# Optimization experiments

Measured on AMD Instinct MI355X. Metric: run time of the kernel, lower is better.

Reference implementation:

```python
import jax, jax.numpy as jnp
import numpy as np
import math

D_MODEL = 192
D_STATE = 16
D_CONV = 3
D_INNER = 2 * D_MODEL
DT_RANK = math.ceil(D_MODEL / 16)  # 12
BATCH, HH, WW = 8, 48, 48
DT_MIN, DT_MAX = 1e-3, 1e-1
EPS = 1e-5


def setup_inputs() -> dict:
    key = jax.random.key(0)
    ks = jax.random.split(key, 10)
    x = jax.random.normal(ks[0], (BATCH, D_MODEL, HH, WW), dtype=jnp.float32)
    in_proj_w = jax.random.normal(ks[1], (2 * D_INNER, D_MODEL), dtype=jnp.float32) * (D_MODEL ** -0.5)
    conv_w = jax.random.normal(ks[2], (D_INNER, 1, D_CONV, D_CONV), dtype=jnp.float32) * (1.0 / 3.0)
    conv_b = jnp.zeros((D_INNER,), dtype=jnp.float32)
    x_proj_w = jax.random.normal(ks[3], (DT_RANK + 2 * D_STATE, D_INNER), dtype=jnp.float32) * (D_INNER ** -0.5)
    dt_std = DT_RANK ** -0.5
    dt_proj_w = jax.random.uniform(ks[4], (D_INNER, DT_RANK), dtype=jnp.float32, minval=-dt_std, maxval=dt_std)
    u = jax.random.uniform(ks[5], (D_INNER,), dtype=jnp.float32)
    dt_proj_b = jnp.exp(u * (math.log(DT_MAX) - math.log(DT_MIN)) + math.log(DT_MIN))
    A_log = jnp.log(jnp.tile(jnp.arange(1, D_STATE + 1, dtype=jnp.float32)[None, :], (D_INNER, 1)))
    D_param = jnp.ones((D_INNER,), dtype=jnp.float32)
    ln_g = jnp.ones((D_INNER,), dtype=jnp.float32)
    ln_b = jnp.zeros((D_INNER,), dtype=jnp.float32)
    out_proj_w = jax.random.normal(ks[6], (D_MODEL, D_INNER), dtype=jnp.float32) * (D_INNER ** -0.5)
    fuse_w = jax.random.normal(ks[7], (D_MODEL, D_MODEL, 1, 1), dtype=jnp.float32) * (D_MODEL ** -0.5)
    fuse_b = jnp.zeros((D_MODEL,), dtype=jnp.float32)
    return dict(x=x, in_proj_w=in_proj_w, conv_w=conv_w, conv_b=conv_b,
                x_proj_w=x_proj_w, dt_proj_w=dt_proj_w, dt_proj_b=dt_proj_b,
                A_log=A_log, D_param=D_param, ln_g=ln_g, ln_b=ln_b,
                out_proj_w=out_proj_w, fuse_w=fuse_w, fuse_b=fuse_b)


def _silu(v):
    return v * jax.nn.sigmoid(v)


def _selective_scan(u, delta, A, Bp, Cp, D_param):
    # u, delta: [B, L, Di]; A: [Di, Ds]; Bp, Cp: [B, L, Ds]; D_param: [Di]
    deltaA = jnp.exp(delta[..., None] * A)                    # [B, L, Di, Ds]
    deltaBu = (delta * u)[..., None] * Bp[:, :, None, :]      # [B, L, Di, Ds]
    a_seq = jnp.moveaxis(deltaA, 1, 0)                        # [L, B, Di, Ds]
    b_seq = jnp.moveaxis(deltaBu, 1, 0)
    c_seq = jnp.moveaxis(Cp, 1, 0)                            # [L, B, Ds]

    def step(h, abc):
        a_t, b_t, c_t = abc
        h = a_t * h + b_t                                     # [B, Di, Ds]
        y = jnp.einsum('bds,bs->bd', h, c_t)                  # [B, Di]
        return h, y

    h0 = jnp.zeros(u.shape[:1] + (u.shape[2], A.shape[1]), dtype=u.dtype)
    _, ys = jax.lax.scan(step, h0, (a_seq, b_seq, c_seq))     # ys: [L, B, Di]
    return jnp.moveaxis(ys, 0, 1) + u * D_param               # [B, L, Di]


def reference(x, in_proj_w, conv_w, conv_b, x_proj_w, dt_proj_w, dt_proj_b,
              A_log, D_param, ln_g, ln_b, out_proj_w, fuse_w, fuse_b):
    Bn, C, H, W = x.shape
    L = H * W
    x_hwc = jnp.transpose(x, (0, 2, 3, 1))                    # [B, H, W, C]
    xz = jnp.einsum('bhwc,oc->bhwo', x_hwc, in_proj_w)        # [B, H, W, 2*Di]
    xin, z = jnp.split(xz, 2, axis=-1)
    xin_c = jnp.transpose(xin, (0, 3, 1, 2))                  # [B, Di, H, W]
    conv = jax.lax.conv_general_dilated(
        xin_c, conv_w, window_strides=(1, 1), padding='SAME',
        feature_group_count=D_INNER,
        dimension_numbers=('NCHW', 'OIHW', 'NCHW')) + conv_b[None, :, None, None]
    xact = _silu(conv)
    x_flat = jnp.transpose(xact.reshape(Bn, D_INNER, L), (0, 2, 1))  # [B, L, Di]
    xp = jnp.einsum('bld,od->blo', x_flat, x_proj_w)          # [B, L, dt_rank+2*Ds]
    dt_low = xp[..., :DT_RANK]
    Bp = xp[..., DT_RANK:DT_RANK + D_STATE]                   # [B, L, Ds]
    Cp = xp[..., DT_RANK + D_STATE:]                          # [B, L, Ds]
    dt = jnp.einsum('blr,dr->bld', dt_low, dt_proj_w)         # [B, L, Di]
    delta = jax.nn.softplus(dt + dt_proj_b)
    A = -jnp.exp(A_log)
    y = _selective_scan(x_flat, delta, A, Bp, Cp, D_param)    # [B, L, Di]
    out = y.reshape(Bn, H, W, D_INNER)
    mu = out.mean(axis=-1, keepdims=True)
    var = out.var(axis=-1, keepdims=True)
    out = (out - mu) * jax.lax.rsqrt(var + EPS) * ln_g + ln_b
    out = out * _silu(z)
    out = jnp.einsum('bhwd,od->bhwo', out, out_proj_w)        # [B, H, W, d_model]
    out_c = jnp.transpose(out, (0, 3, 1, 2))                  # [B, d_model, H, W]
    fused = jnp.einsum('bchw,oc->bohw', out_c, fuse_w[:, :, 0, 0]) + fuse_b[None, :, None, None]
    m = fused.mean(axis=(2, 3), keepdims=True)
    v = fused.var(axis=(2, 3), keepdims=True)
    normed = (fused - m) * jax.lax.rsqrt(v + EPS)             # InstanceNorm2d, no affine
    return x + normed
```

## Files before the change

kernel.cpp:

```cpp
#include <hip/hip_runtime.h>
#include <math.h>

#define B_ 8
#define DM 192
#define DI 384
#define DS 16
#define DTR 12
#define NP 44
#define H_ 48
#define W_ 48
#define L_ (H_*W_)
#define NR (B_*L_)
#define EPS_ 1e-5f
#define CH 96
#define CL 24

typedef unsigned int u32;
typedef unsigned short u16;
typedef _Float16 f16;
typedef _Float16 f16x8 __attribute__((ext_vector_type(8)));
typedef float f32x4 __attribute__((ext_vector_type(4)));

__device__ __forceinline__ u16 f2h(float f) {
  f16 h = (f16)f;
  return __builtin_bit_cast(u16, h);
}
__device__ __forceinline__ float h2f(u16 u) {
  f16 h = __builtin_bit_cast(f16, u);
  return (float)h;
}
__device__ __forceinline__ u32 pack2h(float a, float b) {
  return (u32)f2h(a) | ((u32)f2h(b) << 16);
}

__global__ __launch_bounds__(384) void k_prep(const float* __restrict__ x,
                                              const float* __restrict__ in_w,
                                              const float* __restrict__ xproj_w,
                                              const float* __restrict__ outp_w,
                                              const float* __restrict__ fuse_w,
                                              u16* __restrict__ xT,
                                              u16* __restrict__ Wi,
                                              u16* __restrict__ Wx,
                                              u16* __restrict__ Wc) {
  __shared__ float tile[32][33];
  const int bid = blockIdx.x;
  const int tid = threadIdx.x;
  if (bid < 192) {
    const int o = bid, c = tid;
    float acc = 0.f;
    #pragma unroll 4
    for (int n = 0; n < DM; ++n)
      acc += fuse_w[o*DM + n] * outp_w[(size_t)n*DI + c];
    Wc[(size_t)o*DI + c] = f2h(acc);
  } else if (bid < 3648) {
    const int t = bid - 192;
    const int c0 = (t % 6)*32, l0 = ((t/6) % 72)*32, b = t/(6*72);
    for (int e = tid; e < 1024; e += 384) {
      int ci = e >> 5, li = e & 31;
      tile[ci][li] = x[((size_t)b*DM + c0+ci)*L_ + l0+li];
    }
    __syncthreads();
    for (int e = tid; e < 1024; e += 384) {
      int li = e >> 5, ci = e & 31;
      xT[((size_t)b*L_ + l0+li)*DM + c0+ci] = f2h(tile[ci][li]);
    }
  } else if (bid < 3744) {
    const int q = (bid - 3648)*384 + tid;
    const float4 v = *(const float4*)(in_w + (size_t)q*4);
    u32* dst = (u32*)(Wi + (size_t)q*4);
    dst[0] = pack2h(v.x, v.y);
    dst[1] = pack2h(v.z, v.w);
  } else {
    const int q = (bid - 3744)*384 + tid;
    const float4 v = *(const float4*)(xproj_w + (size_t)q*4);
    u32* dst = (u32*)(Wx + (size_t)q*4);
    dst[0] = pack2h(v.x, v.y);
    dst[1] = pack2h(v.z, v.w);
  }
}

template<int TM, int TN, int KT, int MODE>
__global__ __launch_bounds__(256) void k_tgemm(const u16* __restrict__ A, int lda,
                                               const u16* __restrict__ W, int N,
                                               void* __restrict__ outA,
                                               void* __restrict__ outB,
                                               const float* __restrict__ bias) {
  constexpr int K = KT*32;
  constexpr int WM = TM/2, WN = TN/2;
  constexpr int MT = WM/16, NT = WN/16;
  __shared__ u16 As[TM*72];
  __shared__ u16 Bs[TN*72];
  const int tid = threadIdx.x;
  const int n0 = blockIdx.x * TN;
  const int r0 = blockIdx.y * TM;
  const int lane = tid & 63;
  const int wave = tid >> 6;
  const int wm = (wave & 1) * WM, wn = (wave >> 1) * WN;
  const int lrow = lane & 15, lq = lane >> 4;
  f32x4 acc[MT][NT] = {};
  for (int k0 = 0; k0 < K; k0 += 64) {
    for (int i = tid; i < TM*8; i += 256) {
      int row = i >> 3, seg = i & 7;
      f16x8 v = *(const f16x8*)(A + (size_t)(r0+row)*lda + k0 + seg*8);
      *(f16x8*)&As[row*72 + seg*8] = v;
    }
    for (int i = tid; i < TN*8; i += 256) {
      int row = i >> 3, seg = i & 7;
      int n = n0 + row;
      f16x8 v = {};
      if (n < N) v = *(const f16x8*)(W + (size_t)n*K + k0 + seg*8);
      *(f16x8*)&Bs[row*72 + seg*8] = v;
    }
    __syncthreads();
    #pragma unroll
    for (int kk = 0; kk < 2; ++kk) {
      f16x8 af[MT], bfr[NT];
      #pragma unroll
      for (int t = 0; t < MT; ++t)
        af[t] = *(const f16x8*)&As[(wm + t*16 + lrow)*72 + kk*32 + lq*8];
      #pragma unroll
      for (int t = 0; t < NT; ++t)
        bfr[t] = *(const f16x8*)&Bs[(wn + t*16 + lrow)*72 + kk*32 + lq*8];
      #pragma unroll
      for (int tm = 0; tm < MT; ++tm)
        #pragma unroll
        for (int tn = 0; tn < NT; ++tn)
          acc[tm][tn] = __builtin_amdgcn_mfma_f32_16x16x32_f16(af[tm], bfr[tn], acc[tm][tn], 0, 0, 0);
    }
    __syncthreads();
  }
  #pragma unroll
  for (int tm = 0; tm < MT; ++tm) {
    const int mb = r0 + wm + tm*16 + lq*4;
    #pragma unroll
    for (int tn = 0; tn < NT; ++tn) {
      const int col = n0 + wn + tn*16 + lrow;
      if (MODE == 0) {
        if (col < DI) {
          u16* o = (u16*)outA;
          #pragma unroll
          for (int i = 0; i < 4; ++i) o[(size_t)(mb+i)*DI + col] = f2h(acc[tm][tn][i]);
        } else {
          u16* o = (u16*)outB;
          #pragma unroll
          for (int i = 0; i < 4; ++i) o[(size_t)(mb+i)*DI + (col-DI)] = f2h(acc[tm][tn][i]);
        }
      } else if (MODE == 1) {
        if (col < N) {
          float* o = (float*)outA;
          #pragma unroll
          for (int i = 0; i < 4; ++i) o[(size_t)(mb+i)*NP + col] = acc[tm][tn][i];
        }
      } else {
        u16* o = (u16*)outA;
        const int bb = r0 / L_;
        const int ll = (r0 % L_) + wm + tm*16 + lq*4;
        const float bv = bias[col];
        u16 res[4];
        #pragma unroll
        for (int i = 0; i < 4; ++i) res[i] = f2h(acc[tm][tn][i] + bv);
        *(uint2*)(o + ((size_t)bb*DM + col)*L_ + ll) =
            make_uint2((u32)res[0] | ((u32)res[1] << 16),
                       (u32)res[2] | ((u32)res[3] << 16));
      }
    }
  }
}

__global__ __launch_bounds__(256) void k_conv_silu(const u16* __restrict__ xin,
                                                   const float* __restrict__ cw,
                                                   const float* __restrict__ cb,
                                                   u16* __restrict__ xact) {
  int idx = blockIdx.x*256 + threadIdx.x;
  int cg = idx % 48;
  int pos = idx / 48;
  int w = pos % W_; int h = (pos / W_) % H_; int b = pos / L_;
  int c8 = cg*8;
  float wv[72];
  const float4* wp = (const float4*)(cw + (size_t)c8*9);
  #pragma unroll
  for (int i = 0; i < 18; ++i) {
    float4 t4 = wp[i];
    wv[i*4]=t4.x; wv[i*4+1]=t4.y; wv[i*4+2]=t4.z; wv[i*4+3]=t4.w;
  }
  float acc[8];
  {
    const float4* cbp = (const float4*)(cb + c8);
    float4 b0 = cbp[0], b1 = cbp[1];
    acc[0]=b0.x; acc[1]=b0.y; acc[2]=b0.z; acc[3]=b0.w;
    acc[4]=b1.x; acc[5]=b1.y; acc[6]=b1.z; acc[7]=b1.w;
  }
  #pragma unroll
  for (int dh = -1; dh <= 1; ++dh) {
    int hh = h + dh; if (hh < 0 || hh >= H_) continue;
    #pragma unroll
    for (int dw = -1; dw <= 1; ++dw) {
      int w2 = w + dw; if (w2 < 0 || w2 >= W_) continue;
      int j = (dh+1)*3 + (dw+1);
      const uint4 q = *(const uint4*)(xin + ((size_t)b*L_ + hh*W_ + w2)*DI + c8);
      float v[8];
      v[0]=h2f((u16)(q.x & 0xFFFF)); v[1]=h2f((u16)(q.x >> 16));
      v[2]=h2f((u16)(q.y & 0xFFFF)); v[3]=h2f((u16)(q.y >> 16));
      v[4]=h2f((u16)(q.z & 0xFFFF)); v[5]=h2f((u16)(q.z >> 16));
      v[6]=h2f((u16)(q.w & 0xFFFF)); v[7]=h2f((u16)(q.w >> 16));
      #pragma unroll
      for (int i = 0; i < 8; ++i) acc[i] += v[i]*wv[i*9+j];
    }
  }
  u32 res[4];
  #pragma unroll
  for (int i = 0; i < 4; ++i) {
    float a0 = acc[2*i],   s0 = a0 / (1.f + __expf(-a0));
    float a1 = acc[2*i+1], s1 = a1 / (1.f + __expf(-a1));
    res[i] = pack2h(s0, s1);
  }
  *(uint4*)(xact + (size_t)pos*DI + c8) = make_uint4(res[0], res[1], res[2], res[3]);
}


__global__ __launch_bounds__(128) void k_scan_A(const u16* __restrict__ u,
                                                const float* __restrict__ xp,
                                                const float* __restrict__ dtw,
                                                const float* __restrict__ dtb,
                                                u16* __restrict__ Pb,
                                                u16* __restrict__ hLb) {
  const int tid = threadIdx.x;
  const int d = blockIdx.x*128 + tid;
  const int b = blockIdx.y, c = blockIdx.z;
  const size_t rbase = (size_t)b*L_ + (size_t)c*CL;
  float wr[12];
  #pragma unroll
  for (int k = 0; k < 12; ++k) wr[k] = dtw[d*DTR + k];
  const float bd = dtb[d];
  float h[16] = {};
  float sdlt = 0.f;
  u16 uraw = u[rbase*DI + d];
  for (int j = 0; j < CL; ++j) {
    float uu = h2f(uraw);
    if (j+1 < CL) uraw = u[(rbase+j+1)*DI + d];
    const float* xr = xp + (rbase+j)*NP;
    float dt = bd;
    #pragma unroll
    for (int k = 0; k < 12; ++k) dt += xr[k]*wr[k];
    float dlt = (dt > 20.f) ? dt : __logf(1.f + __expf(dt));
    sdlt += dlt;
    float du = dlt*uu;
    float r = __expf(-dlt);
    float a = r;
    #pragma unroll
    for (int s = 0; s < 16; ++s) {
      h[s] = a*h[s] + du*xr[12+s];
      a *= r;
    }
  }
  float rt = __expf(-sdlt);
  const size_t o = (((size_t)c*B_ + b)*DI + d)*DS;
  u32 pk[8];
  float p1 = rt, p2;
  #pragma unroll
  for (int k = 0; k < 8; ++k) { p2 = p1*rt; pk[k] = pack2h(p1, p2); p1 = p2*rt; }
  *(uint4*)&Pb[o]   = make_uint4(pk[0], pk[1], pk[2], pk[3]);
  *(uint4*)&Pb[o+8] = make_uint4(pk[4], pk[5], pk[6], pk[7]);
  #pragma unroll
  for (int k = 0; k < 8; ++k) pk[k] = pack2h(h[2*k], h[2*k+1]);
  *(uint4*)&hLb[o]   = make_uint4(pk[0], pk[1], pk[2], pk[3]);
  *(uint4*)&hLb[o+8] = make_uint4(pk[4], pk[5], pk[6], pk[7]);
}

__global__ __launch_bounds__(256) void k_scan_B(const u16* __restrict__ Pb,
                                                const u16* __restrict__ hLb,
                                                u16* __restrict__ Sb) {
  const size_t gid = (size_t)blockIdx.x*256 + threadIdx.x;
  float run = 0.f;
  #pragma unroll 8
  for (int c = 0; c < CH; ++c) {
    size_t o = (size_t)c*(B_*DI*DS) + gid;
    Sb[o] = f2h(run);
    run = h2f(Pb[o])*run + h2f(hLb[o]);
  }
}

__global__ __launch_bounds__(384) void k_scan_C(const u16* __restrict__ u,
                                                const float* __restrict__ xp,
                                                const float* __restrict__ dtw,
                                                const float* __restrict__ dtb,
                                                const float* __restrict__ Dp,
                                                const u16* __restrict__ Sb,
                                                const u16* __restrict__ z,
                                                const float* __restrict__ g,
                                                const float* __restrict__ be,
                                                u16* __restrict__ t) {
  __shared__ u16 sy[CL][392];
  __shared__ float smv[CL][2];
  const int tid = threadIdx.x;
  const int b = blockIdx.x, c = blockIdx.y;
  const size_t rbase = (size_t)b*L_ + (size_t)c*CL;
  float wr[12];
  #pragma unroll
  for (int k = 0; k < 12; ++k) wr[k] = dtw[tid*DTR + k];
  const float bd = dtb[tid];
  const float Dpar = Dp[tid];
  const float gd = g[tid], bed = be[tid];
  float h[16];
  {
    const size_t o = (((size_t)c*B_ + b)*DI + tid)*DS;
    uint4 q0 = *(const uint4*)&Sb[o];
    uint4 q1 = *(const uint4*)&Sb[o+8];
    const u32 qs[8] = {q0.x,q0.y,q0.z,q0.w,q1.x,q1.y,q1.z,q1.w};
    #pragma unroll
    for (int k = 0; k < 8; ++k) {
      h[2*k]   = h2f((u16)(qs[k] & 0xFFFF));
      h[2*k+1] = h2f((u16)(qs[k] >> 16));
    }
  }
  u16 uraw = u[rbase*DI + tid];
  for (int j = 0; j < CL; ++j) {
    float uu = h2f(uraw);
    if (j+1 < CL) uraw = u[(rbase+j+1)*DI + tid];
    const float* xr = xp + (rbase+j)*NP;
    float dt = bd;
    #pragma unroll
    for (int k = 0; k < 12; ++k) dt += xr[k]*wr[k];
    float dlt = (dt > 20.f) ? dt : __logf(1.f + __expf(dt));
    float du = dlt*uu;
    float r = __expf(-dlt);
    float a = r;
    float yv = uu * Dpar;
    #pragma unroll
    for (int s = 0; s < 16; ++s) {
      h[s] = a*h[s] + du*xr[12+s];
      yv += h[s]*xr[28+s];
      a *= r;
    }
    sy[j][tid] = f2h(yv);
  }
  __syncthreads();
  {
    const int row = tid >> 4, p = tid & 15;
    float s = 0.f, q = 0.f;
    #pragma unroll
    for (int k = 0; k < 24; ++k) {
      float v = h2f(sy[row][p + 16*k]);
      s += v; q += v*v;
    }
    #pragma unroll
    for (int m = 1; m < 16; m <<= 1) { s += __shfl_xor(s, m); q += __shfl_xor(q, m); }
    if (p == 0) {
      float mu = s * (1.f/DI);
      float var = q * (1.f/DI) - mu*mu;
      smv[row][0] = mu;
      smv[row][1] = rsqrtf(var + EPS_);
    }
  }
  __syncthreads();
  for (int j = 0; j < CL; ++j) {
    float mu = smv[j][0], rstd = smv[j][1];
    float yv = h2f(sy[j][tid]);
    float zz = h2f(z[(rbase+j)*DI + tid]);
    float sz = zz / (1.f + __expf(-zz));
    t[(rbase+j)*DI + tid] = f2h(((yv - mu)*rstd*gd + bed) * sz);
  }
}

__global__ __launch_bounds__(256) void k_inorm(const u16* __restrict__ fused,
                                               const float* __restrict__ x,
                                               float* __restrict__ out) {
  const int bo = blockIdx.x;
  const int tid = threadIdx.x;
  const u16* row = fused + (size_t)bo*L_;
  float s = 0.f, q = 0.f;
  float vr[9];
  #pragma unroll
  for (int k = 0; k < 9; ++k) {
    float v = h2f(row[tid + k*256]);
    vr[k] = v; s += v; q += v*v;
  }
  #pragma unroll
  for (int m = 1; m < 64; m <<= 1) { s += __shfl_xor(s, m); q += __shfl_xor(q, m); }
  __shared__ float ps[4], pq[4];
  if ((tid&63)==0) { ps[tid>>6]=s; pq[tid>>6]=q; }
  __syncthreads();
  float S = ps[0]+ps[1]+ps[2]+ps[3];
  float Q = pq[0]+pq[1]+pq[2]+pq[3];
  float mu = S/(float)L_;
  float var = Q/(float)L_ - mu*mu;
  float rstd = rsqrtf(var + EPS_);
  #pragma unroll
  for (int k = 0; k < 9; ++k) {
    size_t idx = (size_t)bo*L_ + tid + k*256;
    out[idx] = x[idx] + (vr[k]-mu)*rstd;
  }
}

extern "C" void kernel_launch(void* const* d_in, const int* in_sizes, int n_in,
                              void* d_out, int out_size, void* d_ws, size_t ws_size,
                              hipStream_t stream) {
  const float* x       = (const float*)d_in[0];
  const float* in_w    = (const float*)d_in[1];
  const float* conv_w  = (const float*)d_in[2];
  const float* conv_b  = (const float*)d_in[3];
  const float* xproj_w = (const float*)d_in[4];
  const float* dt_w    = (const float*)d_in[5];
  const float* dt_b    = (const float*)d_in[6];
  const float* D_par   = (const float*)d_in[8];
  const float* ln_g    = (const float*)d_in[9];
  const float* ln_bb   = (const float*)d_in[10];
  const float* outp_w  = (const float*)d_in[11];
  const float* fuse_w  = (const float*)d_in[12];
  const float* fuse_b  = (const float*)d_in[13];
  float* out = (float*)d_out;

  float* ws = (float*)d_ws;
  const size_t o_xT    = 0;
  const size_t o_xin   = 1769472;
  const size_t o_z     = 5308416;
  const size_t o_xact  = 8847360;
  const size_t o_xp    = 12386304;
  const size_t o_Wc    = 13197312;
  const size_t o_Wi    = 13234176;
  const size_t o_Wx    = 13307904;
  const size_t o_Pb    = 13316352;
  const size_t o_hL    = 15675648;
  const size_t o_Sb    = 18034944;

  u16*   xT    = (u16*)(ws + o_xT);
  u16*   xin   = (u16*)(ws + o_xin);
  u16*   zb    = (u16*)(ws + o_z);
  u16*   xact  = (u16*)(ws + o_xact);
  float* xp    = ws + o_xp;
  u16*   Wc    = (u16*)(ws + o_Wc);
  u16*   Wi    = (u16*)(ws + o_Wi);
  u16*   Wx    = (u16*)(ws + o_Wx);
  u16*   Pb    = (u16*)(ws + o_Pb);
  u16*   hLb   = (u16*)(ws + o_hL);
  u16*   Sb    = (u16*)(ws + o_Sb);
  u16*   tbuf  = (u16*)(ws + o_Pb);
  u16*   fused = (u16*)(ws + o_Sb);

  k_prep<<<3755, 384, 0, stream>>>(x, in_w, xproj_w, outp_w, fuse_w, xT, Wi, Wx, Wc);
  k_tgemm<64,128,6,0><<<dim3(6,288), 256, 0, stream>>>(xT, DM, Wi, 2*DI, xin, zb, nullptr);
  k_conv_silu<<<NR*48/256, 256, 0, stream>>>(xin, conv_w, conv_b, xact);
  k_tgemm<32,64,12,1><<<dim3(1,576), 256, 0, stream>>>(xact, DI, Wx, NP, xp, nullptr, nullptr);
  k_scan_A<<<dim3(DI/128, B_, CH), 128, 0, stream>>>(xact, xp, dt_w, dt_b, Pb, hLb);
  k_scan_B<<<(B_*DI*DS)/256, 256, 0, stream>>>(Pb, hLb, Sb);
  k_scan_C<<<dim3(B_, CH), 384, 0, stream>>>(xact, xp, dt_w, dt_b, D_par, Sb, zb, ln_g, ln_bb, tbuf);
  k_tgemm<32,64,12,3><<<dim3(3,576), 256, 0, stream>>>(tbuf, DI, Wc, DM, fused, nullptr, fuse_b);
  k_inorm<<<B_*DM, 256, 0, stream>>>(fused, x, out);
}
```

Baseline: 247.3 us.

## Fuse chunk-carry scan into scan_A via last-blocks atomic ticket, share softplus exp

Merges the chunk-state carry pass (formerly k_scan_B) into k_scan_A. Each block takes a ticket from a global atomic counter, and the last 128 blocks spin until all blocks finish, then each runs the sequential carry across chunks for 384 state elements. This removes one kernel launch and its drain gap, but puts the carry on only 128 blocks and relies on an atomic counter reset with a memset. The softplus is also rewritten so the decay exp(-delta) comes from a reciprocal of 1+exp(dt), saving one exp per step.

```diff
diff --git a/kernel.cpp b/kernel.cpp
--- a/kernel.cpp
+++ b/kernel.cpp
@@ -14,6 +14,8 @@
 #define EPS_ 1e-5f
 #define CH 96
 #define CL 24
+#define TOTB (3*B_*CH)
+#define NSPIN 128
 
 typedef unsigned int u32;
 typedef unsigned short u16;
@@ -31,6 +33,15 @@
 }
 __device__ __forceinline__ u32 pack2h(float a, float b) {
   return (u32)f2h(a) | ((u32)f2h(b) << 16);
+}
+
+__device__ __forceinline__ void softplus_decay(float dt, float& dlt, float& r) {
+  if (dt > 20.f) { dlt = dt; r = __expf(-dt); }
+  else {
+    float e = __expf(dt);
+    r = __builtin_amdgcn_rcpf(1.f + e);
+    dlt = -__logf(r);
+  }
 }
 
 __global__ __launch_bounds__(384) void k_prep(const float* __restrict__ x,
@@ -218,12 +229,14 @@
 }
 
 
-__global__ __launch_bounds__(128) void k_scan_A(const u16* __restrict__ u,
-                                                const float* __restrict__ xp,
-                                                const float* __restrict__ dtw,
-                                                const float* __restrict__ dtb,
-                                                u16* __restrict__ Pb,
-                                                u16* __restrict__ hLb) {
+__global__ __launch_bounds__(128) void k_scan_AB(const u16* __restrict__ u,
+                                                 const float* __restrict__ xp,
+                                                 const float* __restrict__ dtw,
+                                                 const float* __restrict__ dtb,
+                                                 u16* __restrict__ Pb,
+                                                 u16* __restrict__ hLb,
+                                                 u16* __restrict__ Sb,
+                                                 u32* __restrict__ counter) {
   const int tid = threadIdx.x;
   const int d = blockIdx.x*128 + tid;
   const int b = blockIdx.y, c = blockIdx.z;
@@ -242,10 +255,10 @@
     float dt = bd;
     #pragma unroll
     for (int k = 0; k < 12; ++k) dt += xr[k]*wr[k];
-    float dlt = (dt > 20.f) ? dt : __logf(1.f + __expf(dt));
+    float dlt, r;
+    softplus_decay(dt, dlt, r);
     sdlt += dlt;
     float du = dlt*uu;
-    float r = __expf(-dlt);
     float a = r;
     #pragma unroll
     for (int s = 0; s < 16; ++s) {
@@ -265,18 +278,29 @@
   for (int k = 0; k < 8; ++k) pk[k] = pack2h(h[2*k], h[2*k+1]);
   *(uint4*)&hLb[o]   = make_uint4(pk[0], pk[1], pk[2], pk[3]);
   *(uint4*)&hLb[o+8] = make_uint4(pk[4], pk[5], pk[6], pk[7]);
-}
-
-__global__ __launch_bounds__(256) void k_scan_B(const u16* __restrict__ Pb,
-                                                const u16* __restrict__ hLb,
-                                                u16* __restrict__ Sb) {
-  const size_t gid = (size_t)blockIdx.x*256 + threadIdx.x;
-  float run = 0.f;
-  #pragma unroll 8
-  for (int c = 0; c < CH; ++c) {
-    size_t o = (size_t)c*(B_*DI*DS) + gid;
-    Sb[o] = f2h(run);
-    run = h2f(Pb[o])*run + h2f(hLb[o]);
+
+  __threadfence();
+  __shared__ u32 sticket;
+  if (tid == 0) sticket = atomicAdd(counter, 1u);
+  __syncthreads();
+  const u32 ticket = sticket;
+  if (ticket < (u32)(TOTB - NSPIN)) return;
+  if (tid == 0) {
+    while (atomicAdd(counter, 0u) < (u32)TOTB) { }
+  }
+  __syncthreads();
+  __threadfence();
+  const u32 slice = ticket - (u32)(TOTB - NSPIN);
+  const size_t g0 = (size_t)slice*384 + tid;
+  float run0 = 0.f, run1 = 0.f, run2 = 0.f;
+  for (int c2 = 0; c2 < CH; ++c2) {
+    const size_t base = (size_t)c2*(B_*DI*DS);
+    Sb[base+g0]     = f2h(run0);
+    Sb[base+g0+128] = f2h(run1);
+    Sb[base+g0+256] = f2h(run2);
+    run0 = h2f(Pb[base+g0])    *run0 + h2f(hLb[base+g0]);
+    run1 = h2f(Pb[base+g0+128])*run1 + h2f(hLb[base+g0+128]);
+    run2 = h2f(Pb[base+g0+256])*run2 + h2f(hLb[base+g0+256]);
   }
 }
 
@@ -321,9 +345,9 @@
     float dt = bd;
     #pragma unroll
     for (int k = 0; k < 12; ++k) dt += xr[k]*wr[k];
-    float dlt = (dt > 20.f) ? dt : __logf(1.f + __expf(dt));
+    float dlt, r;
+    softplus_decay(dt, dlt, r);
     float du = dlt*uu;
-    float r = __expf(-dlt);
     float a = r;
     float yv = uu * Dpar;
     #pragma unroll
@@ -422,6 +446,7 @@
   const size_t o_Pb    = 13316352;
   const size_t o_hL    = 15675648;
   const size_t o_Sb    = 18034944;
+  const size_t o_cnt   = 20394240;
 
   u16*   xT    = (u16*)(ws + o_xT);
   u16*   xin   = (u16*)(ws + o_xin);
@@ -434,15 +459,16 @@
   u16*   Pb    = (u16*)(ws + o_Pb);
   u16*   hLb   = (u16*)(ws + o_hL);
   u16*   Sb    = (u16*)(ws + o_Sb);
+  u32*   cnt   = (u32*)(ws + o_cnt);
   u16*   tbuf  = (u16*)(ws + o_Pb);
   u16*   fused = (u16*)(ws + o_Sb);
 
+  hipMemsetAsync(cnt, 0, sizeof(u32), stream);
   k_prep<<<3755, 384, 0, stream>>>(x, in_w, xproj_w, outp_w, fuse_w, xT, Wi, Wx, Wc);
   k_tgemm<64,128,6,0><<<dim3(6,288), 256, 0, stream>>>(xT, DM, Wi, 2*DI, xin, zb, nullptr);
   k_conv_silu<<<NR*48/256, 256, 0, stream>>>(xin, conv_w, conv_b, xact);
   k_tgemm<32,64,12,1><<<dim3(1,576), 256, 0, stream>>>(xact, DI, Wx, NP, xp, nullptr, nullptr);
-  k_scan_A<<<dim3(DI/128, B_, CH), 128, 0, stream>>>(xact, xp, dt_w, dt_b, Pb, hLb);
-  k_scan_B<<<(B_*DI*DS)/256, 256, 0, stream>>>(Pb, hLb, Sb);
+  k_scan_AB<<<dim3(DI/128, B_, CH), 128, 0, stream>>>(xact, xp, dt_w, dt_b, Pb, hLb, Sb, cnt);
   k_scan_C<<<dim3(B_, CH), 384, 0, stream>>>(xact, xp, dt_w, dt_b, D_par, Sb, zb, ln_g, ln_bb, tbuf);
   k_tgemm<32,64,12,3><<<dim3(3,576), 256, 0, stream>>>(tbuf, DI, Wc, DM, fused, nullptr, fuse_b);
   k_inorm<<<B_*DM, 256, 0, stream>>>(fused, x, out);
```

Measured after the change: 433.2 us. 1.75x slower.
